# Kernel optimization log

Hardware: AMD Instinct MI355X
Metric: run time of the kernel (lower is better)

Reference implementation:

```python
import jax, jax.numpy as jnp
import numpy as np

B, P, ED, AD, DD, E, V, T = 64, 196, 2048, 512, 512, 300, 1000, 96


def setup_inputs() -> dict:
    key = jax.random.key(0)
    ks = jax.random.split(key, 24)
    s = 0.02  # small init scale for weights
    lens = jax.random.randint(ks[2], (B,), 2, T + 1).astype(jnp.int32)
    lens = lens.at[0].set(T)  # ensure max(decode_lengths) == T-1 (static)
    return {
        'encoder_out': jax.random.normal(ks[0], (B, P, ED), jnp.float32),
        'encoded_captions': jax.random.randint(ks[1], (B, T), 0, V),
        'caption_lengths': lens,
        'emb': jax.random.uniform(ks[3], (V, E), jnp.float32, -0.1, 0.1),
        'W_enc_att': jax.random.normal(ks[4], (ED, AD), jnp.float32) * s,
        'b_enc_att': jnp.zeros((AD,), jnp.float32),
        'W_dec_att': jax.random.normal(ks[5], (DD, AD), jnp.float32) * s,
        'b_dec_att': jnp.zeros((AD,), jnp.float32),
        'w_full': jax.random.normal(ks[6], (AD,), jnp.float32) * s,
        'b_full': jnp.zeros((), jnp.float32),
        'W_init_h': jax.random.normal(ks[7], (ED, DD), jnp.float32) * s,
        'b_init_h': jnp.zeros((DD,), jnp.float32),
        'W_init_c': jax.random.normal(ks[8], (ED, DD), jnp.float32) * s,
        'b_init_c': jnp.zeros((DD,), jnp.float32),
        'W_fbeta': jax.random.normal(ks[9], (DD, ED), jnp.float32) * s,
        'b_fbeta': jnp.zeros((ED,), jnp.float32),
        'W_ih': jax.random.normal(ks[10], (E + ED, 4 * DD), jnp.float32) * s,
        'b_ih': jnp.zeros((4 * DD,), jnp.float32),
        'W_hh': jax.random.normal(ks[11], (DD, 4 * DD), jnp.float32) * s,
        'b_hh': jnp.zeros((4 * DD,), jnp.float32),
        'W_fc': jax.random.uniform(ks[12], (DD, V), jnp.float32, -0.1, 0.1),
        'b_fc': jnp.zeros((V,), jnp.float32),
    }


def reference(encoder_out, encoded_captions, caption_lengths, emb,
              W_enc_att, b_enc_att, W_dec_att, b_dec_att, w_full, b_full,
              W_init_h, b_init_h, W_init_c, b_init_c, W_fbeta, b_fbeta,
              W_ih, b_ih, W_hh, b_hh, W_fc, b_fc):
    # Sort by caption length, descending (stable like torch.sort on ints)
    sort_ind = jnp.argsort(-caption_lengths)
    lens = caption_lengths[sort_ind]
    eo = encoder_out[sort_ind]                  # [B,P,ED]
    caps = encoded_captions[sort_ind]           # [B,T]
    decode_lengths = lens - 1                   # [B]

    embs = emb[caps]                            # [B,T,E]
    mean_eo = eo.mean(axis=1)                   # [B,ED]
    h0 = mean_eo @ W_init_h + b_init_h          # [B,DD]
    c0 = mean_eo @ W_init_c + b_init_c

    # encoder-side attention projection is step-invariant: hoist it
    att1 = eo @ W_enc_att + b_enc_att           # [B,P,AD]

    Tdec = T - 1
    ts = jnp.arange(Tdec)
    masks = (decode_lengths[None, :] > ts[:, None]).astype(eo.dtype)  # [Tdec,B]
    emb_seq = jnp.swapaxes(embs[:, :Tdec, :], 0, 1)                    # [Tdec,B,E]

    def step(carry, xs):
        h, c = carry
        emb_t, m = xs                           # [B,E], [B]
        mb = m[:, None]
        # Bahdanau attention
        att2 = h @ W_dec_att + b_dec_att        # [B,AD]
        e = jnp.einsum('bpa,a->bp', jax.nn.relu(att1 + att2[:, None, :]), w_full) + b_full
        alpha = jax.nn.softmax(e, axis=1)       # [B,P]
        awe = jnp.einsum('bpd,bp->bd', eo, alpha)  # [B,ED]
        gate = jax.nn.sigmoid(h @ W_fbeta + b_fbeta)
        x = jnp.concatenate([emb_t, gate * awe], axis=1)  # [B,E+ED]
        # LSTMCell (torch gate order: i, f, g, o)
        gates = x @ W_ih + b_ih + h @ W_hh + b_hh
        i, f, g, o = jnp.split(gates, 4, axis=1)
        c_new = jax.nn.sigmoid(f) * c + jax.nn.sigmoid(i) * jnp.tanh(g)
        h_new = jax.nn.sigmoid(o) * jnp.tanh(c_new)
        # only active rows (sorted so they are a prefix) update state
        h2 = mb * h_new + (1.0 - mb) * h
        c2 = mb * c_new + (1.0 - mb) * c
        preds = (h2 @ W_fc + b_fc) * mb         # dropout = identity (eval)
        return (h2, c2), (preds, alpha * mb)

    (_, _), (preds, alphas) = jax.lax.scan(step, (h0, c0), (emb_seq, masks))
    predictions = jnp.swapaxes(preds, 0, 1)     # [B,Tdec,V]
    alphas = jnp.swapaxes(alphas, 0, 1)         # [B,Tdec,P]
    return predictions, caps, decode_lengths, alphas, sort_ind
```

## Files before the change

kernel.cpp:

```cpp
#include <hip/hip_runtime.h>
#include <stddef.h>
#include <math.h>

static constexpr int B = 64, P = 196, ED = 2048, AD = 512, DD = 512, E = 300, V = 1000, T = 96, TD = 95;
static constexpr int KX = E + ED;
static constexpr int KTOT = KX + DD;
static constexpr int KSPLIT = 8;
static constexpr int KPER = 368;
static constexpr int NG = 4 * DD;

static constexpr size_t POFF   = 0;
static constexpr size_t CAPOFF = (size_t)B * TD * V;
static constexpr size_t DLOFF  = CAPOFF + (size_t)B * T;
static constexpr size_t AOFF   = DLOFF + B;
static constexpr size_t SOFF   = AOFF + (size_t)B * TD * P;

__device__ __forceinline__ float sigm(float x) { return 1.0f / (1.0f + expf(-x)); }

__global__ __launch_bounds__(64) void k_sort(const int* __restrict__ lens,
                                             const int* __restrict__ caps_in,
                                             int* __restrict__ sidx,
                                             int* __restrict__ dlen,
                                             int* __restrict__ caps_s,
                                             float* __restrict__ out) {
    __shared__ int sl[B];
    __shared__ int ss[B];
    int i = threadIdx.x;
    sl[i] = lens[i];
    __syncthreads();
    int li = sl[i];
    int r = 0;
    for (int j = 0; j < B; j++) {
        int lj = sl[j];
        r += (lj > li) || (lj == li && j < i);
    }
    ss[r] = i;
    sidx[r] = i;
    dlen[r] = li - 1;
    out[DLOFF + r] = (float)(li - 1);
    out[SOFF + r] = (float)i;
    __syncthreads();
    for (int idx = i; idx < B * T; idx += B) {
        int b = idx / T, tt = idx % T;
        int v = caps_in[ss[b] * T + tt];
        caps_s[idx] = v;
        out[CAPOFF + idx] = (float)v;
    }
}

__global__ __launch_bounds__(256) void k_mean(const float* __restrict__ eo,
                                              const int* __restrict__ sidx,
                                              float* __restrict__ mean_eo) {
    int b = blockIdx.y;
    int d = blockIdx.x * 256 + threadIdx.x;
    const float* base = eo + ((size_t)sidx[b] * P) * ED + d;
    float s = 0.f;
    for (int p = 0; p < P; p++) s += base[(size_t)p * ED];
    mean_eo[(size_t)b * ED + d] = s * (1.0f / (float)P);
}

__global__ __launch_bounds__(256) void k_init(const float* __restrict__ mean_eo,
                                              const float* __restrict__ Wh, const float* __restrict__ bh,
                                              const float* __restrict__ Wc, const float* __restrict__ bc,
                                              float* __restrict__ h, float* __restrict__ c,
                                              float* __restrict__ xT) {
    int idx = blockIdx.x * 256 + threadIdx.x;
    int b = idx >> 9, j = idx & 511;
    const float* m = mean_eo + (size_t)b * ED;
    float ah = bh[j], ac = bc[j];
    for (int k = 0; k < ED; k++) {
        float mv = m[k];
        ah += mv * Wh[(size_t)k * DD + j];
        ac += mv * Wc[(size_t)k * DD + j];
    }
    h[idx] = ah;
    c[idx] = ac;
    xT[(size_t)(KX + j) * B + b] = ah;
}

__global__ __launch_bounds__(256) void k_att1(const float* __restrict__ eo,
                                              const float* __restrict__ W,
                                              const float* __restrict__ bias,
                                              const int* __restrict__ sidx,
                                              float* __restrict__ att1) {
    int m0 = blockIdx.x * 64, n0 = blockIdx.y * 64;
    __shared__ float sA[16][68];
    __shared__ float sB[16][68];
    int tid = threadIdx.x;
    int tx = tid & 15, ty = tid >> 4;
    float acc[4][4] = {};

    int la_m = tid >> 2;
    int la_k = (tid & 3) * 4;
    int lb_k = tid >> 4;
    int lb_n = (tid & 15) * 4;

    int mA = m0 + la_m;
    int bA = mA / P, pA = mA % P;
    const float* arow = eo + ((size_t)sidx[bA] * P + pA) * ED;

    for (int k0 = 0; k0 < ED; k0 += 16) {
        float4 av = *(const float4*)(arow + k0 + la_k);
        sA[la_k + 0][la_m] = av.x;
        sA[la_k + 1][la_m] = av.y;
        sA[la_k + 2][la_m] = av.z;
        sA[la_k + 3][la_m] = av.w;
        float4 bv = *(const float4*)(W + (size_t)(k0 + lb_k) * AD + n0 + lb_n);
        *(float4*)&sB[lb_k][lb_n] = bv;
        __syncthreads();
#pragma unroll
        for (int kk = 0; kk < 16; kk++) {
            float4 a4 = *(const float4*)&sA[kk][ty * 4];
            float4 b4 = *(const float4*)&sB[kk][tx * 4];
            float av_[4] = {a4.x, a4.y, a4.z, a4.w};
            float bv_[4] = {b4.x, b4.y, b4.z, b4.w};
#pragma unroll
            for (int i = 0; i < 4; i++)
#pragma unroll
                for (int j = 0; j < 4; j++) acc[i][j] += av_[i] * bv_[j];
        }
        __syncthreads();
    }
#pragma unroll
    for (int i = 0; i < 4; i++) {
        int m = m0 + ty * 4 + i;
        int n = n0 + tx * 4;
        float4 o;
        o.x = acc[i][0] + bias[n + 0];
        o.y = acc[i][1] + bias[n + 1];
        o.z = acc[i][2] + bias[n + 2];
        o.w = acc[i][3] + bias[n + 3];
        *(float4*)(att1 + (size_t)m * AD + n) = o;
    }
}

__global__ __launch_bounds__(256) void k_attpred(const float* __restrict__ h,
                                                 const float* __restrict__ att1,
                                                 const float* __restrict__ Wd,
                                                 const float* __restrict__ bd,
                                                 const float* __restrict__ wf,
                                                 const float* __restrict__ bfv,
                                                 const float* __restrict__ Wfc,
                                                 const float* __restrict__ bfc,
                                                 const int* __restrict__ dlen,
                                                 float* __restrict__ alpha,
                                                 float* __restrict__ out,
                                                 int t, int npred) {
    int bid = blockIdx.x;
    int tid = threadIdx.x;
    if (bid < npred) {
        int idx = bid * 256 + tid;
        if (idx < B * V) {
            int b = idx / V, v = idx - b * V;
            const float* hr = h + (size_t)b * DD;
            float acc = bfc[v];
            for (int k = 0; k < DD; k++) acc += hr[k] * Wfc[(size_t)k * V + v];
            bool m = dlen[b] > t;
            out[POFF + ((size_t)b * TD + t) * V + v] = m ? acc : 0.f;
        }
        return;
    }
    int t1 = t + 1;
    if (t1 >= TD) return;
    int b = bid - npred;
    __shared__ float shh[DD];
    __shared__ float sa2[AD];
    __shared__ float swf[AD];
    __shared__ float se[P];
    __shared__ float red[256];

    shh[tid] = h[(size_t)b * DD + tid];
    shh[tid + 256] = h[(size_t)b * DD + tid + 256];
    swf[tid] = wf[tid];
    swf[tid + 256] = wf[tid + 256];
    __syncthreads();

    for (int a = tid; a < AD; a += 256) {
        float acc = bd[a];
        for (int k = 0; k < DD; k++) acc += shh[k] * Wd[(size_t)k * AD + a];
        sa2[a] = acc;
    }
    __syncthreads();

    int w = tid >> 6, lane = tid & 63;
    float bf0 = bfv[0];
    for (int p = w; p < P; p += 4) {
        const float* row = att1 + ((size_t)b * P + p) * AD + lane * 8;
        float4 u0 = *(const float4*)row;
        float4 u1 = *(const float4*)(row + 4);
        float4 s0 = *(const float4*)&sa2[lane * 8];
        float4 s1 = *(const float4*)&sa2[lane * 8 + 4];
        float4 w0 = *(const float4*)&swf[lane * 8];
        float4 w1 = *(const float4*)&swf[lane * 8 + 4];
        float acc = fmaxf(u0.x + s0.x, 0.f) * w0.x + fmaxf(u0.y + s0.y, 0.f) * w0.y +
                    fmaxf(u0.z + s0.z, 0.f) * w0.z + fmaxf(u0.w + s0.w, 0.f) * w0.w +
                    fmaxf(u1.x + s1.x, 0.f) * w1.x + fmaxf(u1.y + s1.y, 0.f) * w1.y +
                    fmaxf(u1.z + s1.z, 0.f) * w1.z + fmaxf(u1.w + s1.w, 0.f) * w1.w;
#pragma unroll
        for (int m = 32; m >= 1; m >>= 1) acc += __shfl_xor(acc, m, 64);
        if (lane == 0) se[p] = acc + bf0;
    }
    __syncthreads();

    red[tid] = (tid < P) ? se[tid] : -1e30f;
    __syncthreads();
    for (int s = 128; s > 0; s >>= 1) {
        if (tid < s) red[tid] = fmaxf(red[tid], red[tid + s]);
        __syncthreads();
    }
    float mx = red[0];
    __syncthreads();
    float ex = (tid < P) ? expf(se[tid] - mx) : 0.f;
    red[tid] = ex;
    __syncthreads();
    for (int s = 128; s > 0; s >>= 1) {
        if (tid < s) red[tid] += red[tid + s];
        __syncthreads();
    }
    float inv = 1.0f / red[0];
    if (tid < P) {
        float a = ex * inv;
        alpha[(size_t)b * P + tid] = a;
        float m = (dlen[b] > t1) ? 1.f : 0.f;
        out[AOFF + ((size_t)b * TD + t1) * P + tid] = a * m;
    }
}

__global__ __launch_bounds__(256) void k_awexg(const float* __restrict__ eo,
                                               const int* __restrict__ sidx,
                                               const float* __restrict__ alpha,
                                               const float* __restrict__ hcur,
                                               const float* __restrict__ Wfb,
                                               const float* __restrict__ bfb,
                                               const float* __restrict__ emb,
                                               const int* __restrict__ caps_s,
                                               float* __restrict__ xT, int t) {
    int b = blockIdx.y, ch = blockIdx.x, tid = threadIdx.x;
    if (ch == 8) {
        if (tid < E) {
            int cap = caps_s[b * T + t];
            xT[(size_t)tid * B + b] = emb[(size_t)cap * E + tid];
        }
        return;
    }
    __shared__ float sal[P];
    __shared__ float shh[DD];
    if (tid < P) sal[tid] = alpha[(size_t)b * P + tid];
    shh[tid] = hcur[(size_t)b * DD + tid];
    shh[tid + 256] = hcur[(size_t)b * DD + tid + 256];
    __syncthreads();
    int d = ch * 256 + tid;
    const float* base = eo + ((size_t)sidx[b] * P) * ED + d;
    float aw = 0.f;
    for (int p = 0; p < P; p++) aw += base[(size_t)p * ED] * sal[p];
    float fb = bfb[d];
    for (int k = 0; k < DD; k++) fb += shh[k] * Wfb[(size_t)k * ED + d];
    xT[(size_t)(E + d) * B + b] = sigm(fb) * aw;
}

__global__ __launch_bounds__(256) void k_gates(const float* __restrict__ xT,
                                               const float* __restrict__ Wih,
                                               const float* __restrict__ Whh,
                                               float* __restrict__ part) {
    int bx = blockIdx.x;
    int ks = bx >> 5, nb = bx & 31;
    int n0 = nb * 64;
    int tid = threadIdx.x;
    int tb = tid & 15, tn = tid >> 4;
    __shared__ float sW[16][68];
    float acc[4][4] = {};
    int kbase = ks * KPER;

    for (int tile = 0; tile < 23; tile++) {
        int k0 = kbase + tile * 16;
        {
            int kk = tid >> 4, q = tid & 15;
            int kg = k0 + kk;
            float4 wv = make_float4(0.f, 0.f, 0.f, 0.f);
            if (kg < KX) wv = *(const float4*)&Wih[(size_t)kg * NG + n0 + q * 4];
            else if (kg < KTOT) wv = *(const float4*)&Whh[(size_t)(kg - KX) * NG + n0 + q * 4];
            *(float4*)&sW[kk][q * 4] = wv;
        }
        __syncthreads();
#pragma unroll
        for (int kk = 0; kk < 16; kk++) {
            int kg = k0 + kk;
            float4 xv = make_float4(0.f, 0.f, 0.f, 0.f);
            if (kg < KTOT) xv = *(const float4*)&xT[(size_t)kg * B + tb * 4];
            float4 wv = *(const float4*)&sW[kk][tn * 4];
            acc[0][0] += xv.x * wv.x; acc[0][1] += xv.x * wv.y; acc[0][2] += xv.x * wv.z; acc[0][3] += xv.x * wv.w;
            acc[1][0] += xv.y * wv.x; acc[1][1] += xv.y * wv.y; acc[1][2] += xv.y * wv.z; acc[1][3] += xv.y * wv.w;
            acc[2][0] += xv.z * wv.x; acc[2][1] += xv.z * wv.y; acc[2][2] += xv.z * wv.z; acc[2][3] += xv.z * wv.w;
            acc[3][0] += xv.w * wv.x; acc[3][1] += xv.w * wv.y; acc[3][2] += xv.w * wv.z; acc[3][3] += xv.w * wv.w;
        }
        __syncthreads();
    }
    float* pr = part + (size_t)ks * B * NG;
#pragma unroll
    for (int i = 0; i < 4; i++) {
        int b = tb * 4 + i;
        float4 o = make_float4(acc[i][0], acc[i][1], acc[i][2], acc[i][3]);
        *(float4*)&pr[(size_t)b * NG + n0 + tn * 4] = o;
    }
}

__global__ __launch_bounds__(256) void k_cell(const float* __restrict__ part,
                                              const float* __restrict__ bih,
                                              const float* __restrict__ bhh,
                                              const float* __restrict__ hc,
                                              const float* __restrict__ cc,
                                              const int* __restrict__ dlen,
                                              float* __restrict__ hn,
                                              float* __restrict__ cn,
                                              float* __restrict__ xT, int t) {
    int idx = blockIdx.x * 256 + threadIdx.x;
    int b = idx >> 9, j = idx & 511;
    float gi = bih[j] + bhh[j];
    float gf = bih[DD + j] + bhh[DD + j];
    float gg = bih[2 * DD + j] + bhh[2 * DD + j];
    float go = bih[3 * DD + j] + bhh[3 * DD + j];
#pragma unroll
    for (int s = 0; s < KSPLIT; s++) {
        const float* pr = part + ((size_t)s * B + b) * NG;
        gi += pr[j];
        gf += pr[DD + j];
        gg += pr[2 * DD + j];
        go += pr[3 * DD + j];
    }
    float cold = cc[idx], hold = hc[idx];
    float cnew = sigm(gf) * cold + sigm(gi) * tanhf(gg);
    float hnew = sigm(go) * tanhf(cnew);
    bool m = dlen[b] > t;
    float h2 = m ? hnew : hold;
    float c2 = m ? cnew : cold;
    hn[idx] = h2;
    cn[idx] = c2;
    xT[(size_t)(KX + j) * B + b] = h2;
}

extern "C" void kernel_launch(void* const* d_in, const int* in_sizes, int n_in,
                              void* d_out, int out_size, void* d_ws, size_t ws_size,
                              hipStream_t stream) {
    const float* eo    = (const float*)d_in[0];
    const int*   caps  = (const int*)d_in[1];
    const int*   lens  = (const int*)d_in[2];
    const float* emb   = (const float*)d_in[3];
    const float* Wea   = (const float*)d_in[4];
    const float* bea   = (const float*)d_in[5];
    const float* Wda   = (const float*)d_in[6];
    const float* bda   = (const float*)d_in[7];
    const float* wfull = (const float*)d_in[8];
    const float* bfull = (const float*)d_in[9];
    const float* Wih_  = (const float*)d_in[10];
    const float* bih_  = (const float*)d_in[11];
    const float* Wic   = (const float*)d_in[12];
    const float* bic   = (const float*)d_in[13];
    const float* Wfb   = (const float*)d_in[14];
    const float* bfb   = (const float*)d_in[15];
    const float* Wih   = (const float*)d_in[16];
    const float* bih   = (const float*)d_in[17];
    const float* Whh   = (const float*)d_in[18];
    const float* bhh   = (const float*)d_in[19];
    const float* Wfc   = (const float*)d_in[20];
    const float* bfc   = (const float*)d_in[21];
    float* out = (float*)d_out;

    char* w = (char*)d_ws;
    auto carve = [&](size_t bytes) -> void* {
        void* p = (void*)w;
        w += (bytes + 255) & ~(size_t)255;
        return p;
    };
    int* sidx     = (int*)carve(B * 4);
    int* dlen     = (int*)carve(B * 4);
    int* caps_s   = (int*)carve((size_t)B * T * 4);
    float* mean_eo = (float*)carve((size_t)B * ED * 4);
    float* hb0    = (float*)carve((size_t)B * DD * 4);
    float* hb1    = (float*)carve((size_t)B * DD * 4);
    float* cb0    = (float*)carve((size_t)B * DD * 4);
    float* cb1    = (float*)carve((size_t)B * DD * 4);
    float* att1   = (float*)carve((size_t)B * P * AD * 4);
    float* alpha  = (float*)carve((size_t)B * P * 4);
    float* xT     = (float*)carve((size_t)(KSPLIT * KPER) * B * 4);
    float* part   = (float*)carve((size_t)KSPLIT * B * NG * 4);
    float* hb[2] = {hb0, hb1};
    float* cb[2] = {cb0, cb1};

    k_sort<<<1, 64, 0, stream>>>(lens, caps, sidx, dlen, caps_s, out);
    k_mean<<<dim3(ED / 256, B), 256, 0, stream>>>(eo, sidx, mean_eo);
    k_init<<<(B * DD) / 256, 256, 0, stream>>>(mean_eo, Wih_, bih_, Wic, bic, hb[0], cb[0], xT);
    k_att1<<<dim3((B * P) / 64, AD / 64), 256, 0, stream>>>(eo, Wea, bea, sidx, att1);
    k_attpred<<<64, 256, 0, stream>>>(hb[0], att1, Wda, bda, wfull, bfull, Wfc, bfc,
                                      dlen, alpha, out, -1, 0);

    for (int t = 0; t < TD; t++) {
        float* hc = hb[t & 1];
        float* cc = cb[t & 1];
        float* hn = hb[(t + 1) & 1];
        float* cn = cb[(t + 1) & 1];
        k_awexg<<<dim3(9, B), 256, 0, stream>>>(eo, sidx, alpha, hc, Wfb, bfb, emb, caps_s, xT, t);
        k_gates<<<256, 256, 0, stream>>>(xT, Wih, Whh, part);
        k_cell<<<(B * DD) / 256, 256, 0, stream>>>(part, bih, bhh, hc, cc, dlen, hn, cn, xT, t);
        k_attpred<<<314, 256, 0, stream>>>(hn, att1, Wda, bda, wfull, bfull, Wfc, bfc,
                                           dlen, alpha, out, t, 250);
    }
}
```

Measured before the change: 20.61 ms.

## Restructure decoder step into tiled kernels and batch output projection after loop

Each timestep is split into separate kernels. One runs a tiled GEMM for the attention projection and the f_beta gate from the previous hidden state, replacing the per-batch-row dot products that each read the full weight matrix. The next kernel does the attention softmax and the one after it the weighted encoder sum. The gate GEMM is retiled to 32-column blocks so it launches more blocks, and the vocabulary projection leaves the serial loop. Hidden states are now stored for every step in a sequence buffer, and a single batched tiled GEMM computes all predictions at the end, at the cost of extra launches per step and more workspace.

```diff
diff --git a/kernel.cpp b/kernel.cpp
--- a/kernel.cpp
+++ b/kernel.cpp
@@ -62,7 +62,7 @@
 __global__ __launch_bounds__(256) void k_init(const float* __restrict__ mean_eo,
                                               const float* __restrict__ Wh, const float* __restrict__ bh,
                                               const float* __restrict__ Wc, const float* __restrict__ bc,
-                                              float* __restrict__ h, float* __restrict__ c,
+                                              float* __restrict__ h0, float* __restrict__ c0,
                                               float* __restrict__ xT) {
     int idx = blockIdx.x * 256 + threadIdx.x;
     int b = idx >> 9, j = idx & 511;
@@ -73,8 +73,8 @@
         ah += mv * Wh[(size_t)k * DD + j];
         ac += mv * Wc[(size_t)k * DD + j];
     }
-    h[idx] = ah;
-    c[idx] = ac;
+    h0[idx] = ah;
+    c0[idx] = ac;
     xT[(size_t)(KX + j) * B + b] = ah;
 }
 
@@ -134,52 +134,95 @@
     }
 }
 
-__global__ __launch_bounds__(256) void k_attpred(const float* __restrict__ h,
-                                                 const float* __restrict__ att1,
-                                                 const float* __restrict__ Wd,
-                                                 const float* __restrict__ bd,
-                                                 const float* __restrict__ wf,
-                                                 const float* __restrict__ bfv,
-                                                 const float* __restrict__ Wfc,
-                                                 const float* __restrict__ bfc,
-                                                 const int* __restrict__ dlen,
-                                                 float* __restrict__ alpha,
-                                                 float* __restrict__ out,
-                                                 int t, int npred) {
-    int bid = blockIdx.x;
+__global__ __launch_bounds__(256) void kA1(const float* __restrict__ hprev,
+                                           const float* __restrict__ Wda, const float* __restrict__ bda,
+                                           const float* __restrict__ Wfb, const float* __restrict__ bfb,
+                                           const float* __restrict__ emb,
+                                           const int* __restrict__ caps_s,
+                                           float* __restrict__ att2g,
+                                           float* __restrict__ fg,
+                                           float* __restrict__ xT, int t) {
+    int bx = blockIdx.x;
     int tid = threadIdx.x;
-    if (bid < npred) {
-        int idx = bid * 256 + tid;
-        if (idx < B * V) {
-            int b = idx / V, v = idx - b * V;
-            const float* hr = h + (size_t)b * DD;
-            float acc = bfc[v];
-            for (int k = 0; k < DD; k++) acc += hr[k] * Wfc[(size_t)k * V + v];
-            bool m = dlen[b] > t;
-            out[POFF + ((size_t)b * TD + t) * V + v] = m ? acc : 0.f;
+    if (bx >= 80) {
+        int k0 = (bx - 80) * 60;
+        for (int l = tid; l < 60 * 64; l += 256) {
+            int r = l >> 6, b = l & 63;
+            int k = k0 + r;
+            int cap = caps_s[b * T + t];
+            xT[(size_t)k * B + b] = emb[(size_t)cap * E + k];
         }
         return;
     }
-    int t1 = t + 1;
-    if (t1 >= TD) return;
-    int b = bid - npred;
-    __shared__ float shh[DD];
+    int n0 = bx * 32;
+    bool is_att = (n0 < AD);
+    __shared__ float sH[16][68];
+    __shared__ float sW[16][36];
+    float acc[4][2] = {};
+    int tb = tid & 15, tn = tid >> 4;
+
+    for (int k0 = 0; k0 < DD; k0 += 16) {
+        {
+            int b = tid >> 2, q = tid & 3;
+            float4 hv = *(const float4*)(hprev + (size_t)b * DD + k0 + q * 4);
+            sH[q * 4 + 0][b] = hv.x;
+            sH[q * 4 + 1][b] = hv.y;
+            sH[q * 4 + 2][b] = hv.z;
+            sH[q * 4 + 3][b] = hv.w;
+        }
+        if (tid < 128) {
+            int kk = tid >> 3, nn = (tid & 7) * 4;
+            float4 wv;
+            if (is_att) wv = *(const float4*)(Wda + (size_t)(k0 + kk) * AD + n0 + nn);
+            else        wv = *(const float4*)(Wfb + (size_t)(k0 + kk) * ED + (n0 - AD) + nn);
+            *(float4*)&sW[kk][nn] = wv;
+        }
+        __syncthreads();
+#pragma unroll
+        for (int kk = 0; kk < 16; kk++) {
+            float4 hv = *(const float4*)&sH[kk][tb * 4];
+            float w0 = sW[kk][tn * 2 + 0];
+            float w1 = sW[kk][tn * 2 + 1];
+            acc[0][0] += hv.x * w0; acc[0][1] += hv.x * w1;
+            acc[1][0] += hv.y * w0; acc[1][1] += hv.y * w1;
+            acc[2][0] += hv.z * w0; acc[2][1] += hv.z * w1;
+            acc[3][0] += hv.w * w0; acc[3][1] += hv.w * w1;
+        }
+        __syncthreads();
+    }
+#pragma unroll
+    for (int i = 0; i < 4; i++)
+#pragma unroll
+        for (int j = 0; j < 2; j++) {
+            int b = tb * 4 + i;
+            int n = n0 + tn * 2 + j;
+            float v = acc[i][j];
+            if (is_att) att2g[(size_t)b * AD + n] = v + bda[n];
+            else {
+                int d = n - AD;
+                fg[(size_t)b * ED + d] = sigm(v + bfb[d]);
+            }
+        }
+}
+
+__global__ __launch_bounds__(256) void kA2(const float* __restrict__ att2g,
+                                           const float* __restrict__ att1,
+                                           const float* __restrict__ wf,
+                                           const float* __restrict__ bfv,
+                                           const int* __restrict__ dlen,
+                                           float* __restrict__ alpha,
+                                           float* __restrict__ out, int t) {
+    int b = blockIdx.x;
+    int tid = threadIdx.x;
     __shared__ float sa2[AD];
     __shared__ float swf[AD];
     __shared__ float se[P];
     __shared__ float red[256];
 
-    shh[tid] = h[(size_t)b * DD + tid];
-    shh[tid + 256] = h[(size_t)b * DD + tid + 256];
+    sa2[tid] = att2g[(size_t)b * AD + tid];
+    sa2[tid + 256] = att2g[(size_t)b * AD + tid + 256];
     swf[tid] = wf[tid];
     swf[tid + 256] = wf[tid + 256];
-    __syncthreads();
-
-    for (int a = tid; a < AD; a += 256) {
-        float acc = bd[a];
-        for (int k = 0; k < DD; k++) acc += shh[k] * Wd[(size_t)k * AD + a];
-        sa2[a] = acc;
-    }
     __syncthreads();
 
     int w = tid >> 6, lane = tid & 63;
@@ -221,65 +264,49 @@
     if (tid < P) {
         float a = ex * inv;
         alpha[(size_t)b * P + tid] = a;
-        float m = (dlen[b] > t1) ? 1.f : 0.f;
-        out[AOFF + ((size_t)b * TD + t1) * P + tid] = a * m;
-    }
-}
-
-__global__ __launch_bounds__(256) void k_awexg(const float* __restrict__ eo,
-                                               const int* __restrict__ sidx,
-                                               const float* __restrict__ alpha,
-                                               const float* __restrict__ hcur,
-                                               const float* __restrict__ Wfb,
-                                               const float* __restrict__ bfb,
-                                               const float* __restrict__ emb,
-                                               const int* __restrict__ caps_s,
-                                               float* __restrict__ xT, int t) {
+        float m = (dlen[b] > t) ? 1.f : 0.f;
+        out[AOFF + ((size_t)b * TD + t) * P + tid] = a * m;
+    }
+}
+
+__global__ __launch_bounds__(256) void kB(const float* __restrict__ eo,
+                                          const int* __restrict__ sidx,
+                                          const float* __restrict__ alpha,
+                                          const float* __restrict__ fg,
+                                          float* __restrict__ xT) {
     int b = blockIdx.y, ch = blockIdx.x, tid = threadIdx.x;
-    if (ch == 8) {
-        if (tid < E) {
-            int cap = caps_s[b * T + t];
-            xT[(size_t)tid * B + b] = emb[(size_t)cap * E + tid];
-        }
-        return;
-    }
     __shared__ float sal[P];
-    __shared__ float shh[DD];
     if (tid < P) sal[tid] = alpha[(size_t)b * P + tid];
-    shh[tid] = hcur[(size_t)b * DD + tid];
-    shh[tid + 256] = hcur[(size_t)b * DD + tid + 256];
     __syncthreads();
     int d = ch * 256 + tid;
     const float* base = eo + ((size_t)sidx[b] * P) * ED + d;
     float aw = 0.f;
     for (int p = 0; p < P; p++) aw += base[(size_t)p * ED] * sal[p];
-    float fb = bfb[d];
-    for (int k = 0; k < DD; k++) fb += shh[k] * Wfb[(size_t)k * ED + d];
-    xT[(size_t)(E + d) * B + b] = sigm(fb) * aw;
-}
-
-__global__ __launch_bounds__(256) void k_gates(const float* __restrict__ xT,
-                                               const float* __restrict__ Wih,
-                                               const float* __restrict__ Whh,
-                                               float* __restrict__ part) {
+    xT[(size_t)(E + d) * B + b] = fg[(size_t)b * ED + d] * aw;
+}
+
+__global__ __launch_bounds__(256) void kC(const float* __restrict__ xT,
+                                          const float* __restrict__ Wih,
+                                          const float* __restrict__ Whh,
+                                          float* __restrict__ part) {
     int bx = blockIdx.x;
-    int ks = bx >> 5, nb = bx & 31;
-    int n0 = nb * 64;
+    int ks = bx >> 6, nb = bx & 63;
+    int n0 = nb * 32;
     int tid = threadIdx.x;
     int tb = tid & 15, tn = tid >> 4;
-    __shared__ float sW[16][68];
-    float acc[4][4] = {};
+    __shared__ float sW[16][36];
+    float acc[4][2] = {};
     int kbase = ks * KPER;
 
     for (int tile = 0; tile < 23; tile++) {
         int k0 = kbase + tile * 16;
-        {
-            int kk = tid >> 4, q = tid & 15;
+        if (tid < 128) {
+            int kk = tid >> 3, nn = (tid & 7) * 4;
             int kg = k0 + kk;
             float4 wv = make_float4(0.f, 0.f, 0.f, 0.f);
-            if (kg < KX) wv = *(const float4*)&Wih[(size_t)kg * NG + n0 + q * 4];
-            else if (kg < KTOT) wv = *(const float4*)&Whh[(size_t)(kg - KX) * NG + n0 + q * 4];
-            *(float4*)&sW[kk][q * 4] = wv;
+            if (kg < KX) wv = *(const float4*)&Wih[(size_t)kg * NG + n0 + nn];
+            else if (kg < KTOT) wv = *(const float4*)&Whh[(size_t)(kg - KX) * NG + n0 + nn];
+            *(float4*)&sW[kk][nn] = wv;
         }
         __syncthreads();
 #pragma unroll
@@ -287,32 +314,34 @@
             int kg = k0 + kk;
             float4 xv = make_float4(0.f, 0.f, 0.f, 0.f);
             if (kg < KTOT) xv = *(const float4*)&xT[(size_t)kg * B + tb * 4];
-            float4 wv = *(const float4*)&sW[kk][tn * 4];
-            acc[0][0] += xv.x * wv.x; acc[0][1] += xv.x * wv.y; acc[0][2] += xv.x * wv.z; acc[0][3] += xv.x * wv.w;
-            acc[1][0] += xv.y * wv.x; acc[1][1] += xv.y * wv.y; acc[1][2] += xv.y * wv.z; acc[1][3] += xv.y * wv.w;
-            acc[2][0] += xv.z * wv.x; acc[2][1] += xv.z * wv.y; acc[2][2] += xv.z * wv.z; acc[2][3] += xv.z * wv.w;
-            acc[3][0] += xv.w * wv.x; acc[3][1] += xv.w * wv.y; acc[3][2] += xv.w * wv.z; acc[3][3] += xv.w * wv.w;
+            float w0 = sW[kk][tn * 2 + 0];
+            float w1 = sW[kk][tn * 2 + 1];
+            acc[0][0] += xv.x * w0; acc[0][1] += xv.x * w1;
+            acc[1][0] += xv.y * w0; acc[1][1] += xv.y * w1;
+            acc[2][0] += xv.z * w0; acc[2][1] += xv.z * w1;
+            acc[3][0] += xv.w * w0; acc[3][1] += xv.w * w1;
         }
         __syncthreads();
     }
     float* pr = part + (size_t)ks * B * NG;
 #pragma unroll
-    for (int i = 0; i < 4; i++) {
-        int b = tb * 4 + i;
-        float4 o = make_float4(acc[i][0], acc[i][1], acc[i][2], acc[i][3]);
-        *(float4*)&pr[(size_t)b * NG + n0 + tn * 4] = o;
-    }
-}
-
-__global__ __launch_bounds__(256) void k_cell(const float* __restrict__ part,
-                                              const float* __restrict__ bih,
-                                              const float* __restrict__ bhh,
-                                              const float* __restrict__ hc,
-                                              const float* __restrict__ cc,
-                                              const int* __restrict__ dlen,
-                                              float* __restrict__ hn,
-                                              float* __restrict__ cn,
-                                              float* __restrict__ xT, int t) {
+    for (int i = 0; i < 4; i++)
+#pragma unroll
+        for (int j = 0; j < 2; j++) {
+            int b = tb * 4 + i, n = n0 + tn * 2 + j;
+            pr[(size_t)b * NG + n] = acc[i][j];
+        }
+}
+
+__global__ __launch_bounds__(256) void kD(const float* __restrict__ part,
+                                          const float* __restrict__ bih,
+                                          const float* __restrict__ bhh,
+                                          const float* __restrict__ hprev,
+                                          const float* __restrict__ cc,
+                                          const int* __restrict__ dlen,
+                                          float* __restrict__ hseq_t,
+                                          float* __restrict__ cn,
+                                          float* __restrict__ xT, int t) {
     int idx = blockIdx.x * 256 + threadIdx.x;
     int b = idx >> 9, j = idx & 511;
     float gi = bih[j] + bhh[j];
@@ -327,15 +356,79 @@
         gg += pr[2 * DD + j];
         go += pr[3 * DD + j];
     }
-    float cold = cc[idx], hold = hc[idx];
+    float cold = cc[idx], hold = hprev[idx];
     float cnew = sigm(gf) * cold + sigm(gi) * tanhf(gg);
     float hnew = sigm(go) * tanhf(cnew);
     bool m = dlen[b] > t;
     float h2 = m ? hnew : hold;
     float c2 = m ? cnew : cold;
-    hn[idx] = h2;
+    hseq_t[idx] = h2;
     cn[idx] = c2;
     xT[(size_t)(KX + j) * B + b] = h2;
+}
+
+__global__ __launch_bounds__(256) void k_predsall(const float* __restrict__ hseq,
+                                                  const float* __restrict__ Wfc,
+                                                  const float* __restrict__ bfc,
+                                                  const int* __restrict__ dlen,
+                                                  float* __restrict__ out) {
+    int t = blockIdx.x;
+    int n0 = blockIdx.y * 64;
+    int tid = threadIdx.x;
+    int tx = tid & 15, ty = tid >> 4;
+    __shared__ float sA[16][68];
+    __shared__ float sB[16][68];
+    float acc[4][4] = {};
+    const float* A = hseq + (size_t)t * B * DD;
+
+    for (int k0 = 0; k0 < DD; k0 += 16) {
+        {
+            int b = tid >> 2, q = tid & 3;
+            float4 hv = *(const float4*)(A + (size_t)b * DD + k0 + q * 4);
+            sA[q * 4 + 0][b] = hv.x;
+            sA[q * 4 + 1][b] = hv.y;
+            sA[q * 4 + 2][b] = hv.z;
+            sA[q * 4 + 3][b] = hv.w;
+        }
+        {
+            int kk = tid >> 4, nn = (tid & 15) * 4;
+            int c = n0 + nn;
+            const float* wrow = Wfc + (size_t)(k0 + kk) * V;
+            float4 wv;
+            if (c + 3 < V) wv = *(const float4*)(wrow + c);
+            else {
+                wv.x = (c + 0 < V) ? wrow[c + 0] : 0.f;
+                wv.y = (c + 1 < V) ? wrow[c + 1] : 0.f;
+                wv.z = (c + 2 < V) ? wrow[c + 2] : 0.f;
+                wv.w = (c + 3 < V) ? wrow[c + 3] : 0.f;
+            }
+            *(float4*)&sB[kk][nn] = wv;
+        }
+        __syncthreads();
+#pragma unroll
+        for (int kk = 0; kk < 16; kk++) {
+            float4 a4 = *(const float4*)&sA[kk][ty * 4];
+            float4 b4 = *(const float4*)&sB[kk][tx * 4];
+            float av_[4] = {a4.x, a4.y, a4.z, a4.w};
+            float bv_[4] = {b4.x, b4.y, b4.z, b4.w};
+#pragma unroll
+            for (int i = 0; i < 4; i++)
+#pragma unroll
+                for (int j = 0; j < 4; j++) acc[i][j] += av_[i] * bv_[j];
+        }
+        __syncthreads();
+    }
+#pragma unroll
+    for (int i = 0; i < 4; i++) {
+        int b = ty * 4 + i;
+        bool m = dlen[b] > t;
+#pragma unroll
+        for (int j = 0; j < 4; j++) {
+            int n = n0 + tx * 4 + j;
+            if (n < V)
+                out[POFF + ((size_t)b * TD + t) * V + n] = m ? (acc[i][j] + bfc[n]) : 0.f;
+        }
+    }
 }
 
 extern "C" void kernel_launch(void* const* d_in, const int* in_sizes, int n_in,
@@ -371,37 +464,37 @@
         w += (bytes + 255) & ~(size_t)255;
         return p;
     };
-    int* sidx     = (int*)carve(B * 4);
-    int* dlen     = (int*)carve(B * 4);
-    int* caps_s   = (int*)carve((size_t)B * T * 4);
+    int* sidx      = (int*)carve(B * 4);
+    int* dlen      = (int*)carve(B * 4);
+    int* caps_s    = (int*)carve((size_t)B * T * 4);
     float* mean_eo = (float*)carve((size_t)B * ED * 4);
-    float* hb0    = (float*)carve((size_t)B * DD * 4);
-    float* hb1    = (float*)carve((size_t)B * DD * 4);
-    float* cb0    = (float*)carve((size_t)B * DD * 4);
-    float* cb1    = (float*)carve((size_t)B * DD * 4);
-    float* att1   = (float*)carve((size_t)B * P * AD * 4);
-    float* alpha  = (float*)carve((size_t)B * P * 4);
-    float* xT     = (float*)carve((size_t)(KSPLIT * KPER) * B * 4);
-    float* part   = (float*)carve((size_t)KSPLIT * B * NG * 4);
-    float* hb[2] = {hb0, hb1};
+    float* h0      = (float*)carve((size_t)B * DD * 4);
+    float* cb0     = (float*)carve((size_t)B * DD * 4);
+    float* cb1     = (float*)carve((size_t)B * DD * 4);
+    float* att1    = (float*)carve((size_t)B * P * AD * 4);
+    float* alphaW  = (float*)carve((size_t)B * P * 4);
+    float* att2g   = (float*)carve((size_t)B * AD * 4);
+    float* fg      = (float*)carve((size_t)B * ED * 4);
+    float* xT      = (float*)carve((size_t)KTOT * B * 4);
+    float* part    = (float*)carve((size_t)KSPLIT * B * NG * 4);
+    float* hseq    = (float*)carve((size_t)TD * B * DD * 4);
     float* cb[2] = {cb0, cb1};
 
     k_sort<<<1, 64, 0, stream>>>(lens, caps, sidx, dlen, caps_s, out);
     k_mean<<<dim3(ED / 256, B), 256, 0, stream>>>(eo, sidx, mean_eo);
-    k_init<<<(B * DD) / 256, 256, 0, stream>>>(mean_eo, Wih_, bih_, Wic, bic, hb[0], cb[0], xT);
+    k_init<<<(B * DD) / 256, 256, 0, stream>>>(mean_eo, Wih_, bih_, Wic, bic, h0, cb0, xT);
     k_att1<<<dim3((B * P) / 64, AD / 64), 256, 0, stream>>>(eo, Wea, bea, sidx, att1);
-    k_attpred<<<64, 256, 0, stream>>>(hb[0], att1, Wda, bda, wfull, bfull, Wfc, bfc,
-                                      dlen, alpha, out, -1, 0);
 
     for (int t = 0; t < TD; t++) {
-        float* hc = hb[t & 1];
+        const float* hprev = (t == 0) ? h0 : (hseq + (size_t)(t - 1) * B * DD);
         float* cc = cb[t & 1];
-        float* hn = hb[(t + 1) & 1];
         float* cn = cb[(t + 1) & 1];
-        k_awexg<<<dim3(9, B), 256, 0, stream>>>(eo, sidx, alpha, hc, Wfb, bfb, emb, caps_s, xT, t);
-        k_gates<<<256, 256, 0, stream>>>(xT, Wih, Whh, part);
-        k_cell<<<(B * DD) / 256, 256, 0, stream>>>(part, bih, bhh, hc, cc, dlen, hn, cn, xT, t);
-        k_attpred<<<314, 256, 0, stream>>>(hn, att1, Wda, bda, wfull, bfull, Wfc, bfc,
-                                           dlen, alpha, out, t, 250);
-    }
-}
+        kA1<<<85, 256, 0, stream>>>(hprev, Wda, bda, Wfb, bfb, emb, caps_s, att2g, fg, xT, t);
+        kA2<<<64, 256, 0, stream>>>(att2g, att1, wfull, bfull, dlen, alphaW, out, t);
+        kB<<<dim3(8, B), 256, 0, stream>>>(eo, sidx, alphaW, fg, xT);
+        kC<<<512, 256, 0, stream>>>(xT, Wih, Whh, part);
+        kD<<<(B * DD) / 256, 256, 0, stream>>>(part, bih, bhh, hprev, cc, dlen,
+                                               hseq + (size_t)t * B * DD, cn, xT, t);
+    }
+    k_predsall<<<dim3(TD, 16), 256, 0, stream>>>(hseq, Wfc, bfc, dlen, out);
+}
```

After: 19.47 ms. 1.06x faster.
